# Performance work log

Hardware: AMD Instinct MI355X
Metric: run time of the kernel (lower is better)

The kernel has to match this reference:

```python
import jax, jax.numpy as jnp
import numpy as np

D_MODEL = 1024
NUM_HEADS = 16
D_K = D_MODEL // NUM_HEADS


def setup_inputs() -> dict:
    key = jax.random.key(0)
    ks = jax.random.split(key, 11)
    B, S = 2, 2048
    scale = 1.0 / np.sqrt(D_MODEL)
    inp = {
        "q": jax.random.normal(ks[0], (B, S, D_MODEL), jnp.float32),
        "k": jax.random.normal(ks[1], (B, S, D_MODEL), jnp.float32),
        "v": jax.random.normal(ks[2], (B, S, D_MODEL), jnp.float32),
        "Wq": jax.random.normal(ks[3], (D_MODEL, D_MODEL), jnp.float32) * scale,
        "bq": jnp.zeros((D_MODEL,), jnp.float32),
        "Wk": jax.random.normal(ks[4], (D_MODEL, D_MODEL), jnp.float32) * scale,
        "bk": jnp.zeros((D_MODEL,), jnp.float32),
        "Wv": jax.random.normal(ks[5], (D_MODEL, D_MODEL), jnp.float32) * scale,
        "bv": jnp.zeros((D_MODEL,), jnp.float32),
        "Wo": jax.random.normal(ks[6], (D_MODEL, D_MODEL), jnp.float32) * scale,
        "bo": jnp.zeros((D_MODEL,), jnp.float32),
    }
    return inp


def _split_heads(x):
    B, S, _ = x.shape
    return x.reshape(B, S, NUM_HEADS, D_K).transpose(0, 2, 1, 3)  # [B,H,S,dk]


def reference(q, k, v, Wq, bq, Wk, bk, Wv, bv, Wo, bo):
    Q = _split_heads(q @ Wq.T + bq)  # [B,H,S,dk]
    K = _split_heads(k @ Wk.T + bk)
    V = _split_heads(v @ Wv.T + bv)
    scores = jnp.einsum("bhqd,bhkd->bhqk", Q, K) / jnp.sqrt(jnp.float32(D_K))
    attn = jax.nn.softmax(scores, axis=-1)
    ctx = jnp.einsum("bhqk,bhkd->bhqd", attn, V)  # [B,H,S,dk]
    B, H, S, dk = ctx.shape
    ctx = ctx.transpose(0, 2, 1, 3).reshape(B, S, D_MODEL)
    return ctx @ Wo.T + bo
```

## Files before the change

### kernel.cpp

```cpp
#include <hip/hip_runtime.h>
#include <hip/hip_bf16.h>

typedef unsigned short ushort_t;
typedef __attribute__((ext_vector_type(4))) float f32x4;
typedef __attribute__((ext_vector_type(16))) float f32x16;
typedef __attribute__((ext_vector_type(8))) short short8;
typedef __attribute__((ext_vector_type(4))) unsigned short us4;

#define D_MODEL 1024
#define NHEAD 16
#define DK 64
#define BATCH 2
#define SEQ 2048
#define MTOT 4096
#define EX (MTOT * D_MODEL)
#define EW (D_MODEL * D_MODEL)
#define NROWS (32 * SEQ)

#define MFMA16(a,b,c) __builtin_amdgcn_mfma_f32_16x16x32_bf16((a),(b),(c),0,0,0)
#define MFMA32(a,b,c) __builtin_amdgcn_mfma_f32_32x32x16_bf16((a),(b),(c),0,0,0)

__device__ __forceinline__ ushort_t f2bf(float f){
    union{float f;unsigned u;}c; c.f=f;
    unsigned u=c.u, r=u+0x7FFFu+((u>>16)&1u);
    return (ushort_t)(r>>16);
}
__device__ __forceinline__ unsigned cvtpk_bf(float a, float b){
    float2 t; t.x = a; t.y = b;
    union{ __hip_bfloat162 h; unsigned u; } c;
    c.h = __float22bfloat162_rn(t);
    return c.u;
}
__device__ __forceinline__ void plswap(unsigned &a, unsigned &b){
    asm volatile("v_permlane32_swap_b32 %0, %1" : "+v"(a), "+v"(b));
}
__device__ __forceinline__ void gload16(const ushort_t* g, ushort_t* l){
    __builtin_amdgcn_global_load_lds((const __attribute__((address_space(1))) unsigned*)g,
                                     (__attribute__((address_space(3))) unsigned*)l, 16, 0, 0);
}
__device__ __forceinline__ int xcd_swz(int nwg){
    int s = blockIdx.x;
    return (s & 7) * (nwg >> 3) + (s >> 3);
}

__global__ void cast1(const float* __restrict__ x, ushort_t* __restrict__ y, int n4){
    int i = blockIdx.x*blockDim.x + threadIdx.x, st = gridDim.x*blockDim.x;
    for(; i < n4; i += st){
        f32x4 v = ((const f32x4*)x)[i];
        us4 o; o[0]=f2bf(v[0]); o[1]=f2bf(v[1]); o[2]=f2bf(v[2]); o[3]=f2bf(v[3]);
        ((us4*)y)[i] = o;
    }
}
__global__ void cast3(const float* __restrict__ a, const float* __restrict__ b,
                      const float* __restrict__ c, ushort_t* __restrict__ dst, int n4){
    const float* s = blockIdx.y==0 ? a : (blockIdx.y==1 ? b : c);
    us4* d = (us4*)(dst + (size_t)blockIdx.y * n4 * 4);
    const f32x4* sv = (const f32x4*)s;
    int i = blockIdx.x*blockDim.x + threadIdx.x, st = gridDim.x*blockDim.x;
    for(; i < n4; i += st){
        f32x4 v = sv[i];
        us4 o; o[0]=f2bf(v[0]); o[1]=f2bf(v[1]); o[2]=f2bf(v[2]); o[3]=f2bf(v[3]);
        d[i] = o;
    }
}

__device__ __forceinline__ void gemm_body(
    const ushort_t* __restrict__ A, const ushort_t* __restrict__ Bm,
    const float* __restrict__ bias, float scale, int bm, int bn, int mode,
    void* __restrict__ out,
    ushort_t* As0, ushort_t* As1, ushort_t* Bs0, ushort_t* Bs1)
{
    const int tid = threadIdx.x, lane = tid & 63, wid = tid >> 6;
    const int row0 = bm << 7, col0 = bn << 7;
    const int wrow = (wid >> 1) << 6, wcol = (wid & 1) << 6;
    const int l4 = lane >> 2, lc = (lane & 3) << 3, lr = lane & 15, ko = (lane >> 4) << 3;
    const f32x4 Z4 = {0.f,0.f,0.f,0.f};

    f32x4 acc[4][4];
#pragma unroll
    for(int i=0;i<4;i++)
#pragma unroll
        for(int j=0;j<4;j++) acc[i][j] = Z4;

#define GSTAGE(AS,BS,k0) do{ \
    gload16(A +(size_t)(row0+32*wid   +l4)*D_MODEL+(k0)+lc, (AS)+(2*wid  )*512); \
    gload16(A +(size_t)(row0+32*wid+16+l4)*D_MODEL+(k0)+lc, (AS)+(2*wid+1)*512); \
    gload16(Bm+(size_t)(col0+32*wid   +l4)*D_MODEL+(k0)+lc, (BS)+(2*wid  )*512); \
    gload16(Bm+(size_t)(col0+32*wid+16+l4)*D_MODEL+(k0)+lc, (BS)+(2*wid+1)*512); \
}while(0)
#define GCOMP(AS,BS) do{ \
    short8 af[4], bf[4]; \
    _Pragma("unroll") for(int i=0;i<4;i++) af[i]=*(const short8*)((AS)+(wrow+i*16+lr)*32+ko); \
    _Pragma("unroll") for(int j=0;j<4;j++) bf[j]=*(const short8*)((BS)+(wcol+j*16+lr)*32+ko); \
    __builtin_amdgcn_s_setprio(1); \
    _Pragma("unroll") for(int i=0;i<4;i++) \
    _Pragma("unroll") for(int j=0;j<4;j++) acc[i][j]=MFMA16(af[i],bf[j],acc[i][j]); \
    __builtin_amdgcn_s_setprio(0); \
}while(0)

    GSTAGE(As0,Bs0,0);
    __syncthreads();
#pragma unroll 1
    for(int t=0; t<32; t+=2){
        if(t+1<32) GSTAGE(As1,Bs1,(t+1)*32);
        GCOMP(As0,Bs0);
        __syncthreads();
        if(t+2<32) GSTAGE(As0,Bs0,(t+2)*32);
        GCOMP(As1,Bs1);
        __syncthreads();
    }
#undef GSTAGE
#undef GCOMP

    const int rr4 = (lane >> 4) << 2;
#pragma unroll
    for(int i=0;i<4;i++){
#pragma unroll
        for(int j=0;j<4;j++){
            const int m0 = row0 + wrow + i*16 + rr4;
            const int n  = col0 + wcol + j*16 + lr;
            const float bs = bias[n];
            if(mode == 2){
                float* O = (float*)out;
#pragma unroll
                for(int r=0;r<4;r++) O[(size_t)(m0+r)*D_MODEL+n] = (acc[i][j][r]+bs)*scale;
            } else if(mode == 0){
                ushort_t* O = (ushort_t*)out;
#pragma unroll
                for(int r=0;r<4;r++) O[(size_t)(m0+r)*D_MODEL+n] = f2bf((acc[i][j][r]+bs)*scale);
            } else {
                ushort_t* O = (ushort_t*)out;
                const int bb = m0 >> 11, s = m0 & 2047, h = n >> 6, d = n & 63;
                us4 p;
#pragma unroll
                for(int r=0;r<4;r++) p[r] = f2bf((acc[i][j][r]+bs)*scale);
                *(us4*)(O + ((size_t)(bb*NHEAD + h)*DK + d)*SEQ + s) = p;
            }
        }
    }
}

#define QSCALE (0.125f * 1.44269504088896f)

__global__ __launch_bounds__(256,2)
void qkv_fused(const ushort_t* __restrict__ Xq, const ushort_t* __restrict__ Xk,
               const ushort_t* __restrict__ Xv,
               const ushort_t* __restrict__ Wq, const ushort_t* __restrict__ Wk,
               const ushort_t* __restrict__ Wv,
               const float* __restrict__ bq, const float* __restrict__ bk,
               const float* __restrict__ bv,
               ushort_t* Qp, ushort_t* Kp, ushort_t* VtG)
{
    __shared__ ushort_t As0[4096], As1[4096], Bs0[4096], Bs1[4096];
    const int wk = xcd_swz(768);
    const int which = wk >> 8, t = wk & 255;
    const ushort_t *A, *Bm; const float* bias; float scale; int mode; void* out;
    if(which == 0){ A=Xq; Bm=Wq; bias=bq; scale=QSCALE; mode=0; out=Qp; }
    else if(which == 1){ A=Xk; Bm=Wk; bias=bk; scale=1.f; mode=0; out=Kp; }
    else { A=Xv; Bm=Wv; bias=bv; scale=1.f; mode=1; out=VtG; }
    gemm_body(A,Bm,bias,scale, t>>3, t&7, mode, out, As0,As1,Bs0,Bs1);
}

__global__ __launch_bounds__(256,2)
void gemm_one(const ushort_t* __restrict__ A, const ushort_t* __restrict__ Bm,
              const float* __restrict__ bias, float scale, int mode, void* out)
{
    __shared__ ushort_t As0[4096], As1[4096], Bs0[4096], Bs1[4096];
    const int wk = xcd_swz(256);
    gemm_body(A,Bm,bias,scale, wk>>3, wk&7, mode, out, As0,As1,Bs0,Bs1);
}

__global__ __launch_bounds__(128,2)
void attn_fwd(const ushort_t* __restrict__ Qp, const ushort_t* __restrict__ Kp,
              const ushort_t* __restrict__ VtG, ushort_t* __restrict__ ctx)
{
    __shared__ ushort_t Ks0[64*64], Ks1[64*64];
    __shared__ ushort_t Vs0[64*64], Vs1[64*64];

    const int wk = xcd_swz(1024);
    const int bh = wk >> 5, qt = wk & 31;
    const int b = bh >> 4, h = bh & 15;
    const int tid = threadIdx.x, lane = tid & 63, wid = tid >> 6;
    const int lq = lane & 31, hi = lane >> 5, lx = lq & 7;
    const size_t qkbase = (size_t)b*SEQ*D_MODEL + h*DK;
    const size_t vbase  = (size_t)bh * DK * SEQ;
    const int q0 = qt*64 + wid*32;

    short8 qa[4];
#pragma unroll
    for(int s=0;s<4;s++)
        qa[s] = *(const short8*)(Qp + qkbase + (size_t)(q0+lq)*D_MODEL + s*16 + hi*8);

    f32x16 o[2];
    float run_m = -1e30f, run_l = 0.f;
#pragma unroll
    for(int i=0;i<16;i++){ o[0][i] = 0.f; o[1][i] = 0.f; }

    const int srow = lane >> 3;
    const int jsw  = (((lane & 7) ^ srow) << 3);

#define ASTAGE(KS, VS, kv) do{ \
    _Pragma("unroll") for(int c=0;c<4;c++){ \
        const int rb = wid*32 + c*8; \
        gload16(Kp  + qkbase + (size_t)((kv)+rb+srow)*D_MODEL + jsw, (KS) + rb*64); \
        gload16(VtG + vbase  + (size_t)(rb+srow)*SEQ + (kv) + jsw,   (VS) + rb*64); \
    } \
}while(0)

#define APHASE(KS, VS) do{ \
    f32x16 st0, st1; \
    __builtin_amdgcn_s_setprio(1); \
    { f32x16 acc; \
      _Pragma("unroll") for(int i=0;i<16;i++) acc[i]=0.f; \
      _Pragma("unroll") for(int s=0;s<4;s++){ \
          short8 kf = *(const short8*)((KS) + lq*64 + (((2*s+hi)^lx)<<3)); \
          acc = MFMA32(kf, qa[s], acc); } \
      st0 = acc; } \
    { f32x16 acc; \
      _Pragma("unroll") for(int i=0;i<16;i++) acc[i]=0.f; \
      _Pragma("unroll") for(int s=0;s<4;s++){ \
          short8 kf = *(const short8*)((KS) + (32+lq)*64 + (((2*s+hi)^lx)<<3)); \
          acc = MFMA32(kf, qa[s], acc); } \
      st1 = acc; } \
    __builtin_amdgcn_s_setprio(0); \
    float tr[8]; \
    _Pragma("unroll") for(int i=0;i<8;i++) tr[i] = fmaxf(fmaxf(st0[i],st0[i+8]), fmaxf(st1[i],st1[i+8])); \
    _Pragma("unroll") for(int w=4;w;w>>=1) \
    _Pragma("unroll") for(int i=0;i<w;i++) tr[i]=fmaxf(tr[i],tr[i+w]); \
    const float pmax = fmaxf(tr[0], __shfl_xor(tr[0], 32)); \
    if(__any(pmax > run_m + 8.f)){ \
        const float nm = fmaxf(run_m, pmax); \
        const float corr = exp2f(run_m - nm); \
        run_m = nm; run_l *= corr; \
        _Pragma("unroll") for(int i=0;i<16;i++){ o[0][i]*=corr; o[1][i]*=corr; } \
    } \
    float ts[16]; \
    _Pragma("unroll") for(int i=0;i<16;i++){ \
        st0[i] = exp2f(st0[i] - run_m); \
        st1[i] = exp2f(st1[i] - run_m); \
        ts[i] = st0[i] + st1[i]; } \
    _Pragma("unroll") for(int w=8;w;w>>=1) \
    _Pragma("unroll") for(int i=0;i<w;i++) ts[i]+=ts[i+w]; \
    run_l += ts[0] + __shfl_xor(ts[0], 32); \
    _Pragma("unroll") for(int sub=0; sub<2; sub++){ \
        unsigned w8[8]; \
        _Pragma("unroll") for(int i=0;i<8;i++) \
            w8[i] = cvtpk_bf(sub==0 ? st0[2*i] : st1[2*i], sub==0 ? st0[2*i+1] : st1[2*i+1]); \
        plswap(w8[0], w8[2]); plswap(w8[1], w8[3]); \
        plswap(w8[4], w8[6]); plswap(w8[5], w8[7]); \
        union { unsigned u[4]; short8 s; } p0, p1; \
        p0.u[0]=w8[0]; p0.u[1]=w8[1]; p0.u[2]=w8[2]; p0.u[3]=w8[3]; \
        p1.u[0]=w8[4]; p1.u[1]=w8[5]; p1.u[2]=w8[6]; p1.u[3]=w8[7]; \
        __builtin_amdgcn_s_setprio(1); \
        _Pragma("unroll") for(int ds=0; ds<2; ds++){ \
            short8 v0 = *(const short8*)((VS) + (ds*32+lq)*64 + (((sub*4+0+hi)^lx)<<3)); \
            short8 v1 = *(const short8*)((VS) + (ds*32+lq)*64 + (((sub*4+2+hi)^lx)<<3)); \
            o[ds] = MFMA32(v0, p0.s, o[ds]); \
            o[ds] = MFMA32(v1, p1.s, o[ds]); } \
        __builtin_amdgcn_s_setprio(0); \
    } \
}while(0)

    ASTAGE(Ks0, Vs0, 0);
    __syncthreads();
#pragma unroll 1
    for(int kv0 = 0; kv0 < SEQ; kv0 += 128){
        if(kv0 + 64 < SEQ) ASTAGE(Ks1, Vs1, kv0 + 64);
        APHASE(Ks0, Vs0);
        __syncthreads();
        if(kv0 + 128 < SEQ) ASTAGE(Ks0, Vs0, kv0 + 128);
        APHASE(Ks1, Vs1);
        __syncthreads();
    }
#undef ASTAGE

    const float linv = 1.f / run_l;
#pragma unroll
    for(int ds=0; ds<2; ds++)
#pragma unroll
        for(int g=0; g<4; g++){
            unsigned lo = cvtpk_bf(o[ds][4*g+0]*linv, o[ds][4*g+1]*linv);
            unsigned hi2 = cvtpk_bf(o[ds][4*g+2]*linv, o[ds][4*g+3]*linv);
            union { unsigned u[2]; us4 v; } pp; pp.u[0]=lo; pp.u[1]=hi2;
            *(us4*)(ctx + qkbase + (size_t)(q0+lq)*D_MODEL + ds*32 + 8*g + 4*hi) = pp.v;
        }
}

__global__ __launch_bounds__(128,4)
void attn_split(const ushort_t* __restrict__ Qp, const ushort_t* __restrict__ Kp,
                const ushort_t* __restrict__ VtG,
                float* __restrict__ Op, float* __restrict__ Lp)
{
    __shared__ ushort_t Ks[64*64];
    __shared__ ushort_t Vs[64*64];

    const int wk = xcd_swz(2048);
    const int half = wk & 1, bhqt = wk >> 1;
    const int bh = bhqt >> 5, qt = bhqt & 31;
    const int b = bh >> 4, h = bh & 15;
    const int tid = threadIdx.x, lane = tid & 63, wid = tid >> 6;
    const int lq = lane & 31, hi = lane >> 5, lx = lq & 7;
    const size_t qkbase = (size_t)b*SEQ*D_MODEL + h*DK;
    const size_t vbase  = (size_t)bh * DK * SEQ;
    const int q0 = qt*64 + wid*32;
    const int kvbeg = half * (SEQ/2);

    short8 qa[4];
#pragma unroll
    for(int s=0;s<4;s++)
        qa[s] = *(const short8*)(Qp + qkbase + (size_t)(q0+lq)*D_MODEL + s*16 + hi*8);

    const f32x16 Z16 = {0.f,0.f,0.f,0.f,0.f,0.f,0.f,0.f,0.f,0.f,0.f,0.f,0.f,0.f,0.f,0.f};
    f32x16 o[2];
    float2 run_l2; run_l2.x = 0.f; run_l2.y = 0.f;
    o[0] = Z16; o[1] = Z16;

    const int srow = lane >> 3;
    const int jsw  = (((lane & 7) ^ srow) << 3);

#pragma unroll 1
    for(int kv0 = kvbeg; kv0 < kvbeg + SEQ/2; kv0 += 64){
#pragma unroll
        for(int c=0;c<4;c++){
            const int rb = wid*32 + c*8;
            gload16(Kp  + qkbase + (size_t)(kv0+rb+srow)*D_MODEL + jsw, Ks + rb*64);
            gload16(VtG + vbase  + (size_t)(rb+srow)*SEQ + kv0 + jsw,   Vs + rb*64);
        }
        __syncthreads();

        f32x16 st0, st1;
        __builtin_amdgcn_s_setprio(1);
        {
            f32x16 acc = Z16;
#pragma unroll
            for(int s=0;s<4;s++){
                short8 kf = *(const short8*)(Ks + lq*64 + (((2*s+hi)^lx)<<3));
                acc = MFMA32(kf, qa[s], acc);
            }
            st0 = acc;
        }
        {
            f32x16 acc = Z16;
#pragma unroll
            for(int s=0;s<4;s++){
                short8 kf = *(const short8*)(Ks + (32+lq)*64 + (((2*s+hi)^lx)<<3));
                acc = MFMA32(kf, qa[s], acc);
            }
            st1 = acc;
        }
        __builtin_amdgcn_s_setprio(0);

#pragma unroll
        for(int i=0;i<16;i++){
            st0[i] = exp2f(st0[i]);
            st1[i] = exp2f(st1[i]);
        }
        float2 t2[8];
#pragma unroll
        for(int i=0;i<8;i++){
            t2[i].x = st0[2*i] + st1[2*i];
            t2[i].y = st0[2*i+1] + st1[2*i+1];
        }
#pragma unroll
        for(int w=4;w;w>>=1)
#pragma unroll
            for(int i=0;i<w;i++){ t2[i].x += t2[i+w].x; t2[i].y += t2[i+w].y; }
        run_l2.x += t2[0].x; run_l2.y += t2[0].y;

#pragma unroll
        for(int sub=0; sub<2; sub++){
            unsigned w8[8];
#pragma unroll
            for(int i=0;i<8;i++)
                w8[i] = cvtpk_bf(sub==0 ? st0[2*i] : st1[2*i], sub==0 ? st0[2*i+1] : st1[2*i+1]);
            plswap(w8[0], w8[2]); plswap(w8[1], w8[3]);
            plswap(w8[4], w8[6]); plswap(w8[5], w8[7]);
            union { unsigned u[4]; short8 s; } p0, p1;
            p0.u[0]=w8[0]; p0.u[1]=w8[1]; p0.u[2]=w8[2]; p0.u[3]=w8[3];
            p1.u[0]=w8[4]; p1.u[1]=w8[5]; p1.u[2]=w8[6]; p1.u[3]=w8[7];
            __builtin_amdgcn_s_setprio(1);
#pragma unroll
            for(int ds=0; ds<2; ds++){
                short8 v0 = *(const short8*)(Vs + (ds*32+lq)*64 + (((sub*4+0+hi)^lx)<<3));
                short8 v1 = *(const short8*)(Vs + (ds*32+lq)*64 + (((sub*4+2+hi)^lx)<<3));
                o[ds] = MFMA32(v0, p0.s, o[ds]);
                o[ds] = MFMA32(v1, p1.s, o[ds]);
            }
            __builtin_amdgcn_s_setprio(0);
        }
        __syncthreads();
    }

    float lsum = run_l2.x + run_l2.y;
    lsum += __shfl_xor(lsum, 32);

    const size_t rbase = ((size_t)half*NROWS + (size_t)bh*SEQ + q0 + lq) * 64;
#pragma unroll
    for(int ds=0; ds<2; ds++)
#pragma unroll
        for(int g=0; g<4; g++){
            f32x4 v; v[0]=o[ds][4*g+0]; v[1]=o[ds][4*g+1]; v[2]=o[ds][4*g+2]; v[3]=o[ds][4*g+3];
            *(f32x4*)(Op + rbase + ds*32 + 8*g + 4*hi) = v;
        }
    if(hi == 0)
        Lp[(size_t)half*NROWS + (size_t)bh*SEQ + q0 + lq] = lsum;
}

__global__ void attn_combine(const float* __restrict__ Op, const float* __restrict__ Lp,
                             ushort_t* __restrict__ ctx)
{
    const int lane = threadIdx.x & 63;
    int w = blockIdx.x * (blockDim.x >> 6) + (threadIdx.x >> 6);
    const int nw = gridDim.x * (blockDim.x >> 6);
    for(int row = w; row < NROWS; row += nw){
        float inv = 1.f / (Lp[row] + Lp[NROWS + row]);
        float o0 = Op[(size_t)row*64 + lane];
        float o1 = Op[((size_t)NROWS + row)*64 + lane];
        float o = (o0 + o1) * inv;
        const int bh = row >> 11, q = row & 2047;
        const int b = bh >> 4, h = bh & 15;
        ctx[((size_t)b*SEQ + q)*D_MODEL + h*DK + lane] = f2bf(o);
    }
}

extern "C" void kernel_launch(void* const* d_in, const int* in_sizes, int n_in,
                              void* d_out, int out_size, void* d_ws, size_t ws_size,
                              hipStream_t stream) {
    (void)in_sizes; (void)n_in; (void)out_size;
    const float* q  = (const float*)d_in[0];
    const float* k  = (const float*)d_in[1];
    const float* v  = (const float*)d_in[2];
    const float* Wq = (const float*)d_in[3];
    const float* bq = (const float*)d_in[4];
    const float* Wk = (const float*)d_in[5];
    const float* bk = (const float*)d_in[6];
    const float* Wv = (const float*)d_in[7];
    const float* bv = (const float*)d_in[8];
    const float* Wo = (const float*)d_in[9];
    const float* bo = (const float*)d_in[10];
    float* out = (float*)d_out;

    ushort_t* WS = (ushort_t*)d_ws;
    const dim3 blk(256);
    const int n4x = EX/4, n4w = EW/4;

    const size_t baseA   = (size_t)(6*(size_t)EX + 3*(size_t)EW) * 2;
    const size_t partial = ((size_t)2*NROWS*64 + (size_t)2*NROWS) * 4;

    if(ws_size >= baseA){
        ushort_t* Xq  = WS;
        ushort_t* Xk  = Xq + EX;
        ushort_t* Xv  = Xk + EX;
        ushort_t* Wqb = Xv + EX;
        ushort_t* Wkb = Wqb + EW;
        ushort_t* Wvb = Wkb + EW;
        ushort_t* Qp  = Wvb + EW;
        ushort_t* Kp  = Qp + EX;
        ushort_t* VtG = Kp + EX;
        ushort_t* ctx = Xq;
        ushort_t* Wob = Wqb;

        cast3<<<dim3(1024,3), blk, 0, stream>>>(q, k, v, Xq, n4x);
        cast3<<<dim3(256,3),  blk, 0, stream>>>(Wq, Wk, Wv, Wqb, n4w);
        qkv_fused<<<768, blk, 0, stream>>>(Xq,Xk,Xv, Wqb,Wkb,Wvb, bq,bk,bv, Qp,Kp,VtG);
        cast1<<<512, blk, 0, stream>>>(Wo, Wob, n4w);

        if(ws_size >= baseA + partial){
            float* Op = (float*)(VtG + EX);
            float* Lp = Op + (size_t)2*NROWS*64;
            attn_split<<<2048, dim3(128), 0, stream>>>(Qp, Kp, VtG, Op, Lp);
            attn_combine<<<2048, blk, 0, stream>>>(Op, Lp, ctx);
        } else {
            attn_fwd<<<1024, dim3(128), 0, stream>>>(Qp, Kp, VtG, ctx);
        }
        gemm_one<<<256, blk, 0, stream>>>(ctx, Wob, bo, 1.f, 2, out);
    } else {
        ushort_t* Xb  = WS;
        ushort_t* Wb  = Xb + EX;
        ushort_t* Qp  = Wb + EW;
        ushort_t* Kp  = Qp + EX;
        ushort_t* VtG = Kp + EX;
        ushort_t* ctx = Xb;

        cast1<<<1024, blk, 0, stream>>>(q, Xb, n4x);
        cast1<<<512,  blk, 0, stream>>>(Wq, Wb, n4w);
        gemm_one<<<256, blk, 0, stream>>>(Xb, Wb, bq, QSCALE, 0, Qp);
        cast1<<<1024, blk, 0, stream>>>(k, Xb, n4x);
        cast1<<<512,  blk, 0, stream>>>(Wk, Wb, n4w);
        gemm_one<<<256, blk, 0, stream>>>(Xb, Wb, bk, 1.f, 0, Kp);
        cast1<<<1024, blk, 0, stream>>>(v, Xb, n4x);
        cast1<<<512,  blk, 0, stream>>>(Wv, Wb, n4w);
        gemm_one<<<256, blk, 0, stream>>>(Xb, Wb, bv, 1.f, 1, VtG);
        attn_fwd<<<1024, dim3(128), 0, stream>>>(Qp, Kp, VtG, ctx);
        cast1<<<512, blk, 0, stream>>>(Wo, Wb, n4w);
        gemm_one<<<256, blk, 0, stream>>>(ctx, Wb, bo, 1.f, 2, out);
    }
}
```

Baseline: 152.7 us.

## Fuse fp32-to-bf16 activation cast into QKV GEMM A-operand loading

The QKV projection kernel now reads fp32 q/k/v directly, loads A tiles into registers, converts them to bf16 and writes them to shared memory within the double-buffered loop. This removes the separate activation cast pass and its bf16 round trip through global memory. The four weight casts (including Wo) are merged into one launch. In exchange, the GEMM reads twice as many A bytes and adds register-staged conversion work that may not overlap as well as the async global-to-LDS path.

New measurement: 142.3 us. 1.07x faster.

```diff
diff --git a/kernel.cpp b/kernel.cpp
--- a/kernel.cpp
+++ b/kernel.cpp
@@ -51,9 +51,10 @@
         ((us4*)y)[i] = o;
     }
 }
-__global__ void cast3(const float* __restrict__ a, const float* __restrict__ b,
-                      const float* __restrict__ c, ushort_t* __restrict__ dst, int n4){
-    const float* s = blockIdx.y==0 ? a : (blockIdx.y==1 ? b : c);
+__global__ void cast4(const float* __restrict__ a, const float* __restrict__ b,
+                      const float* __restrict__ c, const float* __restrict__ d4,
+                      ushort_t* __restrict__ dst, int n4){
+    const float* s = blockIdx.y==0 ? a : (blockIdx.y==1 ? b : (blockIdx.y==2 ? c : d4));
     us4* d = (us4*)(dst + (size_t)blockIdx.y * n4 * 4);
     const f32x4* sv = (const f32x4*)s;
     int i = blockIdx.x*blockDim.x + threadIdx.x, st = gridDim.x*blockDim.x;
@@ -110,7 +111,6 @@
         __syncthreads();
     }
 #undef GSTAGE
-#undef GCOMP
 
     const int rr4 = (lane >> 4) << 2;
 #pragma unroll
@@ -138,13 +138,14 @@
             }
         }
     }
+#undef GCOMP
 }
 
 #define QSCALE (0.125f * 1.44269504088896f)
 
 __global__ __launch_bounds__(256,2)
-void qkv_fused(const ushort_t* __restrict__ Xq, const ushort_t* __restrict__ Xk,
-               const ushort_t* __restrict__ Xv,
+void qkv_fused(const float* __restrict__ Xq, const float* __restrict__ Xk,
+               const float* __restrict__ Xv,
                const ushort_t* __restrict__ Wq, const ushort_t* __restrict__ Wk,
                const ushort_t* __restrict__ Wv,
                const float* __restrict__ bq, const float* __restrict__ bk,
@@ -154,11 +155,98 @@
     __shared__ ushort_t As0[4096], As1[4096], Bs0[4096], Bs1[4096];
     const int wk = xcd_swz(768);
     const int which = wk >> 8, t = wk & 255;
-    const ushort_t *A, *Bm; const float* bias; float scale; int mode; void* out;
-    if(which == 0){ A=Xq; Bm=Wq; bias=bq; scale=QSCALE; mode=0; out=Qp; }
-    else if(which == 1){ A=Xk; Bm=Wk; bias=bk; scale=1.f; mode=0; out=Kp; }
-    else { A=Xv; Bm=Wv; bias=bv; scale=1.f; mode=1; out=VtG; }
-    gemm_body(A,Bm,bias,scale, t>>3, t&7, mode, out, As0,As1,Bs0,Bs1);
+    const float *Af; const ushort_t *Bm; const float* bias; float scale; int mode; void* out;
+    if(which == 0){ Af=Xq; Bm=Wq; bias=bq; scale=QSCALE; mode=0; out=Qp; }
+    else if(which == 1){ Af=Xk; Bm=Wk; bias=bk; scale=1.f; mode=0; out=Kp; }
+    else { Af=Xv; Bm=Wv; bias=bv; scale=1.f; mode=1; out=VtG; }
+
+    const int bm = t >> 3, bn = t & 7;
+    const int tid = threadIdx.x, lane = tid & 63, wid = tid >> 6;
+    const int row0 = bm << 7, col0 = bn << 7;
+    const int wrow = (wid >> 1) << 6, wcol = (wid & 1) << 6;
+    const int l4 = lane >> 2, lc = (lane & 3) << 3, lr = lane & 15, ko = (lane >> 4) << 3;
+    const f32x4 Z4 = {0.f,0.f,0.f,0.f};
+
+    f32x4 acc[4][4];
+#pragma unroll
+    for(int i=0;i<4;i++)
+#pragma unroll
+        for(int j=0;j<4;j++) acc[i][j] = Z4;
+
+    f32x4 ar[2][2][2];
+
+#define ALOAD(R, k0) do{ \
+    _Pragma("unroll") for(int c=0;c<2;c++){ \
+        const float* src = Af + (size_t)(row0+32*wid+16*c+l4)*D_MODEL + (k0)+lc; \
+        (R)[c][0] = *(const f32x4*)(src); \
+        (R)[c][1] = *(const f32x4*)(src+4); \
+    } \
+}while(0)
+#define AWRITE(AS, R) do{ \
+    _Pragma("unroll") for(int c=0;c<2;c++){ \
+        union{ unsigned u[4]; short8 s; } P; \
+        P.u[0]=cvtpk_bf((R)[c][0][0],(R)[c][0][1]); \
+        P.u[1]=cvtpk_bf((R)[c][0][2],(R)[c][0][3]); \
+        P.u[2]=cvtpk_bf((R)[c][1][0],(R)[c][1][1]); \
+        P.u[3]=cvtpk_bf((R)[c][1][2],(R)[c][1][3]); \
+        *(short8*)((AS) + (2*wid+c)*512 + lane*8) = P.s; \
+    } \
+}while(0)
+#define BSTAGE(BS,k0) do{ \
+    gload16(Bm+(size_t)(col0+32*wid   +l4)*D_MODEL+(k0)+lc, (BS)+(2*wid  )*512); \
+    gload16(Bm+(size_t)(col0+32*wid+16+l4)*D_MODEL+(k0)+lc, (BS)+(2*wid+1)*512); \
+}while(0)
+#define GCOMP(AS,BS) do{ \
+    short8 af[4], bf[4]; \
+    _Pragma("unroll") for(int i=0;i<4;i++) af[i]=*(const short8*)((AS)+(wrow+i*16+lr)*32+ko); \
+    _Pragma("unroll") for(int j=0;j<4;j++) bf[j]=*(const short8*)((BS)+(wcol+j*16+lr)*32+ko); \
+    __builtin_amdgcn_s_setprio(1); \
+    _Pragma("unroll") for(int i=0;i<4;i++) \
+    _Pragma("unroll") for(int j=0;j<4;j++) acc[i][j]=MFMA16(af[i],bf[j],acc[i][j]); \
+    __builtin_amdgcn_s_setprio(0); \
+}while(0)
+
+    ALOAD(ar[0], 0); BSTAGE(Bs0, 0);
+    AWRITE(As0, ar[0]);
+    __syncthreads();
+#pragma unroll 1
+    for(int t2=0; t2<32; t2+=2){
+        if(t2+1<32){ ALOAD(ar[1], (t2+1)*32); BSTAGE(Bs1, (t2+1)*32); }
+        GCOMP(As0,Bs0);
+        if(t2+1<32) AWRITE(As1, ar[1]);
+        __syncthreads();
+        if(t2+2<32){ ALOAD(ar[0], (t2+2)*32); BSTAGE(Bs0, (t2+2)*32); }
+        GCOMP(As1,Bs1);
+        if(t2+2<32) AWRITE(As0, ar[0]);
+        __syncthreads();
+    }
+#undef ALOAD
+#undef AWRITE
+#undef BSTAGE
+#undef GCOMP
+
+    const int rr4 = (lane >> 4) << 2;
+#pragma unroll
+    for(int i=0;i<4;i++){
+#pragma unroll
+        for(int j=0;j<4;j++){
+            const int m0 = row0 + wrow + i*16 + rr4;
+            const int n  = col0 + wcol + j*16 + lr;
+            const float bs = bias[n];
+            if(mode == 0){
+                ushort_t* O = (ushort_t*)out;
+#pragma unroll
+                for(int r=0;r<4;r++) O[(size_t)(m0+r)*D_MODEL+n] = f2bf((acc[i][j][r]+bs)*scale);
+            } else {
+                ushort_t* O = (ushort_t*)out;
+                const int bb = m0 >> 11, s = m0 & 2047, h = n >> 6, d = n & 63;
+                us4 p;
+#pragma unroll
+                for(int r=0;r<4;r++) p[r] = f2bf((acc[i][j][r]+bs)*scale);
+                *(us4*)(O + ((size_t)(bb*NHEAD + h)*DK + d)*SEQ + s) = p;
+            }
+        }
+    }
 }
 
 __global__ __launch_bounds__(256,2)
@@ -444,29 +532,25 @@
     const dim3 blk(256);
     const int n4x = EX/4, n4w = EW/4;
 
-    const size_t baseA   = (size_t)(6*(size_t)EX + 3*(size_t)EW) * 2;
-    const size_t partial = ((size_t)2*NROWS*64 + (size_t)2*NROWS) * 4;
-
-    if(ws_size >= baseA){
-        ushort_t* Xq  = WS;
-        ushort_t* Xk  = Xq + EX;
-        ushort_t* Xv  = Xk + EX;
-        ushort_t* Wqb = Xv + EX;
+    const size_t tierA2 = ((size_t)4*EW + (size_t)4*EX) * 2
+                        + ((size_t)2*NROWS*64 + (size_t)2*NROWS) * 4;
+    const size_t tierA1 = ((size_t)4*EW + (size_t)4*EX) * 2;
+
+    if(ws_size >= tierA1){
+        ushort_t* Wqb = WS;
         ushort_t* Wkb = Wqb + EW;
         ushort_t* Wvb = Wkb + EW;
-        ushort_t* Qp  = Wvb + EW;
+        ushort_t* Wob = Wvb + EW;
+        ushort_t* Qp  = Wob + EW;
         ushort_t* Kp  = Qp + EX;
         ushort_t* VtG = Kp + EX;
-        ushort_t* ctx = Xq;
-        ushort_t* Wob = Wqb;
-
-        cast3<<<dim3(1024,3), blk, 0, stream>>>(q, k, v, Xq, n4x);
-        cast3<<<dim3(256,3),  blk, 0, stream>>>(Wq, Wk, Wv, Wqb, n4w);
-        qkv_fused<<<768, blk, 0, stream>>>(Xq,Xk,Xv, Wqb,Wkb,Wvb, bq,bk,bv, Qp,Kp,VtG);
-        cast1<<<512, blk, 0, stream>>>(Wo, Wob, n4w);
-
-        if(ws_size >= baseA + partial){
-            float* Op = (float*)(VtG + EX);
+        ushort_t* ctx = VtG + EX;
+
+        cast4<<<dim3(256,4), blk, 0, stream>>>(Wq, Wk, Wv, Wo, Wqb, n4w);
+        qkv_fused<<<768, blk, 0, stream>>>(q, k, v, Wqb, Wkb, Wvb, bq, bk, bv, Qp, Kp, VtG);
+
+        if(ws_size >= tierA2){
+            float* Op = (float*)(ctx + EX);
             float* Lp = Op + (size_t)2*NROWS*64;
             attn_split<<<2048, dim3(128), 0, stream>>>(Qp, Kp, VtG, Op, Lp);
             attn_combine<<<2048, blk, 0, stream>>>(Op, Lp, ctx);
```
